# Kernel tuning notes

Hardware: AMD Instinct MI355X
Metric: run time of the kernel (lower is better)

The kernel has to match this reference:

```python
import jax, jax.numpy as jnp
import numpy as np

MARGIN = 1.0
EPS = 1e-6  # torch F.pairwise_distance default eps
B, C, D = 16384, 1000, 1024


def setup_inputs() -> dict:
    key = jax.random.key(0)
    k1, k2, k3 = jax.random.split(key, 3)
    inputs = jax.random.normal(k1, (B, D), dtype=jnp.float32)
    labels = jax.random.randint(k2, (B,), 0, C, dtype=jnp.int64)
    target = jax.random.normal(k3, (C, D), dtype=jnp.float32)
    return {"inputs": inputs, "labels": labels, "target": target}


def _pairdist(a, b):
    # torch F.pairwise_distance(p=2): ||a - b + eps||_2 along last dim
    d = a - b + EPS
    return jnp.sqrt(jnp.sum(d * d, axis=-1))


def reference(inputs, labels, target):
    # --- negative mining: full [B, C] distance matrix via GEMM identity ---
    # (eps is a uniform per-component shift; it does not change the argmin in practice,
    #  and mining indices are non-differentiable anyway)
    x2 = jnp.sum(inputs * inputs, axis=-1, keepdims=True)          # [B, 1]
    t2 = jnp.sum(target * target, axis=-1)                          # [C]
    d2 = x2 - 2.0 * (inputs @ target.T) + t2[None, :]               # [B, C]
    d2 = jnp.maximum(d2, 0.0)
    # exclude the anchor's own class (tx == anchor_label skipped in torch loop)
    own = jax.nn.one_hot(labels, C, dtype=jnp.bool_)                 # [B, C]
    d2 = jnp.where(own, jnp.inf, d2)
    neg_idx = jnp.argmin(d2, axis=-1)                                # [B]

    positive = target[labels]                                        # [B, D]
    negative = target[neg_idx]                                       # [B, D]

    d_ap = _pairdist(inputs, positive)                               # [B]
    d_an = _pairdist(inputs, negative)                               # [B]
    per_anchor = jnp.maximum(d_ap - d_an + MARGIN, 0.0)
    # every anchor forms a valid triplet (C > 1), so total/valid == mean
    return jnp.mean(per_anchor)
```

## Files before the change

kernel.cpp:

```cpp
#include <hip/hip_runtime.h>
#include <hip/hip_bf16.h>

#define NB 16384
#define NC 1000
#define NCP 1024
#define ND 1024
#define BM 128
#define BN 256
#define KSTEPS 32
#define NCB 4

typedef __attribute__((ext_vector_type(8))) short bf16x8;
typedef __attribute__((ext_vector_type(4))) float f32x4;

typedef __attribute__((address_space(1))) const void GV;
typedef __attribute__((address_space(3))) void LV;

__device__ __forceinline__ unsigned short f2bf(float f) {
  union { float f; unsigned u; } c; c.f = f;
  unsigned b = c.u;
  return (unsigned short)((b + 0x7fffu + ((b >> 16) & 1u)) >> 16);
}
__device__ __forceinline__ unsigned pk2(float lo, float hi) {
  return ((unsigned)f2bf(hi) << 16) | (unsigned)f2bf(lo);
}

__global__ __launch_bounds__(256) void prep_kernel(const float* __restrict__ Tf,
                                                   unsigned short* __restrict__ Tb,
                                                   float* __restrict__ t2) {
  const int c = blockIdx.x;
  const int tid = threadIdx.x;
  if (c >= NC) {
    ushort4 z; z.x = z.y = z.z = z.w = 0;
    ((ushort4*)(Tb + (size_t)c * ND))[tid] = z;
    if (tid == 0) t2[c] = 1e30f;
    return;
  }
  float4 v = ((const float4*)(Tf + (size_t)c * ND))[tid];
  float ss = v.x * v.x + v.y * v.y + v.z * v.z + v.w * v.w;
  ushort4 o;
  o.x = f2bf(v.x); o.y = f2bf(v.y); o.z = f2bf(v.z); o.w = f2bf(v.w);
  ((ushort4*)(Tb + (size_t)c * ND))[tid] = o;
  #pragma unroll
  for (int m = 1; m < 64; m <<= 1) ss += __shfl_xor(ss, m, 64);
  __shared__ float red[4];
  if ((tid & 63) == 0) red[tid >> 6] = ss;
  __syncthreads();
  if (tid == 0) t2[c] = red[0] + red[1] + red[2] + red[3];
}

__global__ __launch_bounds__(256) void prepx_kernel(const float* __restrict__ X,
                                                    unsigned short* __restrict__ Xb,
                                                    float* __restrict__ x2) {
  const int r = blockIdx.x;
  const int tid = threadIdx.x;
  float4 v = ((const float4*)(X + (size_t)r * ND))[tid];
  float ss = v.x * v.x + v.y * v.y + v.z * v.z + v.w * v.w;
  ushort4 o;
  o.x = f2bf(v.x); o.y = f2bf(v.y); o.z = f2bf(v.z); o.w = f2bf(v.w);
  ((ushort4*)(Xb + (size_t)r * ND))[tid] = o;
  #pragma unroll
  for (int m = 1; m < 64; m <<= 1) ss += __shfl_xor(ss, m, 64);
  __shared__ float red[4];
  if ((tid & 63) == 0) red[tid >> 6] = ss;
  __syncthreads();
  if (tid == 0) x2[r] = red[0] + red[1] + red[2] + red[3];
}

__global__ __launch_bounds__(512, 4) void mine4_kernel(
    const unsigned short* __restrict__ Xb, const int* __restrict__ labels,
    const unsigned short* __restrict__ Tb, const float* __restrict__ t2g,
    float* __restrict__ slab, float2* __restrict__ pairs) {
  __shared__ char sA[2][BM * 64];
  __shared__ char sB[2][BN * 64];
  __shared__ int sLab[BM];
  __shared__ float2 sMin[BM][4];

  const int tid = threadIdx.x;
  const int lane = tid & 63;
  const int wid = tid >> 6;
  const int l15 = lane & 15, l4 = lane >> 4;
  const int wr = wid >> 2, wc = wid & 3;

  const int bid = (int)blockIdx.x;
  const int wgid = (bid & 7) * 64 + (bid >> 3);
  const int rb = wgid >> 2, cb = wgid & 3;
  const int rowbase = rb * BM, colbase = cb * BN;

  if (tid < BM) sLab[tid] = labels[rowbase + tid];

  auto stage = [&](int buf, int ks) {
    {
      const int o = tid * 16;
      const char* src = (const char*)Xb + (size_t)(rowbase + (o >> 6)) * 2048 + ks * 64 + (o & 63);
      __builtin_amdgcn_global_load_lds((GV*)src, (LV*)(sA[buf] + o), 16, 0, 0);
    }
    #pragma unroll
    for (int i = 0; i < 2; ++i) {
      const int o = i * 8192 + tid * 16;
      const char* src = (const char*)Tb + (size_t)(colbase + (o >> 6)) * 2048 + ks * 64 + (o & 63);
      __builtin_amdgcn_global_load_lds((GV*)src, (LV*)(sB[buf] + o), 16, 0, 0);
    }
  };

  f32x4 acc[4][4] = {};
  stage(0, 0);
  int cur = 0;
  for (int ks = 0; ks < KSTEPS; ++ks) {
    __syncthreads();
    if (ks + 1 < KSTEPS) stage(cur ^ 1, ks + 1);
    const char* pa = sA[cur];
    const char* pb = sB[cur];
    bf16x8 af[4];
    #pragma unroll
    for (int m = 0; m < 4; ++m)
      af[m] = *(const bf16x8*)(pa + ((wr * 64 + m * 16 + l15) * 64 + l4 * 16));
    #pragma unroll
    for (int n = 0; n < 4; ++n) {
      bf16x8 bfr = *(const bf16x8*)(pb + ((wc * 64 + n * 16 + l15) * 64 + l4 * 16));
      #pragma unroll
      for (int m = 0; m < 4; ++m)
        acc[m][n] = __builtin_amdgcn_mfma_f32_16x16x32_bf16(af[m], bfr, acc[m][n], 0, 0, 0);
    }
    cur ^= 1;
  }

  float t2v[4];
  #pragma unroll
  for (int n = 0; n < 4; ++n) t2v[n] = t2g[colbase + wc * 64 + n * 16 + l15];

  #pragma unroll
  for (int m = 0; m < 4; ++m) {
    #pragma unroll
    for (int j = 0; j < 4; ++j) {
      const int rowl = wr * 64 + m * 16 + l4 * 4 + j;
      const int lab = sLab[rowl];
      float bv = 3.0e38f; int bi = 0x7fffffff;
      #pragma unroll
      for (int n = 0; n < 4; ++n) {
        const int col = colbase + wc * 64 + n * 16 + l15;
        const float sc = t2v[n] - 2.0f * acc[m][n][j];
        if (col == lab) slab[rowbase + rowl] = sc;
        const float sce = (col == lab) ? 3.2e38f : sc;
        if (sce < bv || (sce == bv && col < bi)) { bv = sce; bi = col; }
      }
      #pragma unroll
      for (int mk = 1; mk < 16; mk <<= 1) {
        const float ov = __shfl_xor(bv, mk, 64);
        const int   oi = __shfl_xor(bi, mk, 64);
        if (ov < bv || (ov == bv && oi < bi)) { bv = ov; bi = oi; }
      }
      if (l15 == 0) sMin[rowl][wc] = make_float2(bv, __int_as_float(bi));
    }
  }
  __syncthreads();
  if (tid < BM) {
    float2 p = sMin[tid][0];
    #pragma unroll
    for (int q = 1; q < 4; ++q) {
      float2 o = sMin[tid][q];
      if (o.x < p.x || (o.x == p.x && __float_as_int(o.y) < __float_as_int(p.y))) p = o;
    }
    pairs[(size_t)(rowbase + tid) * NCB + cb] = p;
  }
}

__global__ __launch_bounds__(512, 4) void mine2_kernel(
    const float* __restrict__ X, const int* __restrict__ labels,
    const unsigned short* __restrict__ Tb, const float* __restrict__ t2g,
    float* __restrict__ x2g, float* __restrict__ slab, float2* __restrict__ pairs) {
  __shared__ char sA[2][BM * 64];
  __shared__ char sB[2][BN * 64];
  __shared__ int sLab[BM];
  __shared__ float2 sMin[BM][4];

  const int tid = threadIdx.x;
  const int lane = tid & 63;
  const int wid = tid >> 6;
  const int l15 = lane & 15, l4 = lane >> 4;
  const int wr = wid >> 2, wc = wid & 3;
  const int rb = (int)blockIdx.x >> 2, cb = (int)blockIdx.x & 3;
  const int rowbase = rb * BM, colbase = cb * BN;

  if (tid < BM) sLab[tid] = labels[rowbase + tid];

  const int arow = tid >> 2;
  const float* aptr = X + (size_t)(rowbase + arow) * ND + ((tid & 3) << 3);
  float ss = 0.0f;

  f32x4 acc[4][4] = {};
  int cur = 0;

  auto stage = [&](int buf, int ks) {
    #pragma unroll
    for (int i = 0; i < 2; ++i) {
      const int o = i * 8192 + tid * 16;
      const char* src = (const char*)Tb + (size_t)(colbase + (o >> 6)) * 2048 + ks * 64 + (o & 63);
      __builtin_amdgcn_global_load_lds((GV*)src, (LV*)(sB[buf] + o), 16, 0, 0);
    }
    float4 v0 = *(const float4*)(aptr + ks * 32);
    float4 v1 = *(const float4*)(aptr + ks * 32 + 4);
    if (cb == 0) {
      ss += v0.x * v0.x + v0.y * v0.y + v0.z * v0.z + v0.w * v0.w
          + v1.x * v1.x + v1.y * v1.y + v1.z * v1.z + v1.w * v1.w;
    }
    uint4 w;
    w.x = pk2(v0.x, v0.y); w.y = pk2(v0.z, v0.w);
    w.z = pk2(v1.x, v1.y); w.w = pk2(v1.z, v1.w);
    *(uint4*)(sA[buf] + tid * 16) = w;
  };

  stage(0, 0);
  for (int ks = 0; ks < KSTEPS; ++ks) {
    __syncthreads();
    if (ks + 1 < KSTEPS) stage(cur ^ 1, ks + 1);
    const char* pa = sA[cur];
    const char* pb = sB[cur];
    bf16x8 af[4];
    #pragma unroll
    for (int m = 0; m < 4; ++m)
      af[m] = *(const bf16x8*)(pa + ((wr * 64 + m * 16 + l15) * 64 + l4 * 16));
    #pragma unroll
    for (int n = 0; n < 4; ++n) {
      bf16x8 bfr = *(const bf16x8*)(pb + ((wc * 64 + n * 16 + l15) * 64 + l4 * 16));
      #pragma unroll
      for (int m = 0; m < 4; ++m)
        acc[m][n] = __builtin_amdgcn_mfma_f32_16x16x32_bf16(af[m], bfr, acc[m][n], 0, 0, 0);
    }
    cur ^= 1;
  }

  if (cb == 0) {
    ss += __shfl_xor(ss, 1, 64);
    ss += __shfl_xor(ss, 2, 64);
    if ((tid & 3) == 0) x2g[rowbase + arow] = ss;
  }

  float t2v[4];
  #pragma unroll
  for (int n = 0; n < 4; ++n) t2v[n] = t2g[colbase + wc * 64 + n * 16 + l15];

  #pragma unroll
  for (int m = 0; m < 4; ++m) {
    #pragma unroll
    for (int j = 0; j < 4; ++j) {
      const int rowl = wr * 64 + m * 16 + l4 * 4 + j;
      const int lab = sLab[rowl];
      float bv = 3.0e38f; int bi = 0x7fffffff;
      #pragma unroll
      for (int n = 0; n < 4; ++n) {
        const int col = colbase + wc * 64 + n * 16 + l15;
        const float sc = t2v[n] - 2.0f * acc[m][n][j];
        if (col == lab) slab[rowbase + rowl] = sc;
        const float sce = (col == lab) ? 3.2e38f : sc;
        if (sce < bv || (sce == bv && col < bi)) { bv = sce; bi = col; }
      }
      #pragma unroll
      for (int mk = 1; mk < 16; mk <<= 1) {
        const float ov = __shfl_xor(bv, mk, 64);
        const int   oi = __shfl_xor(bi, mk, 64);
        if (ov < bv || (ov == bv && oi < bi)) { bv = ov; bi = oi; }
      }
      if (l15 == 0) sMin[rowl][wc] = make_float2(bv, __int_as_float(bi));
    }
  }
  __syncthreads();
  if (tid < BM) {
    float2 p = sMin[tid][0];
    #pragma unroll
    for (int q = 1; q < 4; ++q) {
      float2 o = sMin[tid][q];
      if (o.x < p.x || (o.x == p.x && __float_as_int(o.y) < __float_as_int(p.y))) p = o;
    }
    pairs[(size_t)(rowbase + tid) * NCB + cb] = p;
  }
}

__global__ __launch_bounds__(256) void finalize_kernel(
    const float2* __restrict__ pairs, const float* __restrict__ slab,
    const float* __restrict__ x2g, float* __restrict__ out) {
  const int r = blockIdx.x * 256 + threadIdx.x;
  float2 p = pairs[(size_t)r * NCB];
  #pragma unroll
  for (int q = 1; q < NCB; ++q) {
    float2 o = pairs[(size_t)r * NCB + q];
    if (o.x < p.x || (o.x == p.x && __float_as_int(o.y) < __float_as_int(p.y))) p = o;
  }
  const float x2v = x2g[r];
  const float dap = sqrtf(fmaxf(x2v + slab[r], 0.0f));
  const float dan = sqrtf(fmaxf(x2v + p.x, 0.0f));
  float h = fmaxf(dap - dan + 1.0f, 0.0f);
  #pragma unroll
  for (int mk = 1; mk < 64; mk <<= 1) h += __shfl_xor(h, mk, 64);
  __shared__ float red[4];
  if ((threadIdx.x & 63) == 0) red[threadIdx.x >> 6] = h;
  __syncthreads();
  if (threadIdx.x == 0)
    atomicAdd(out, (red[0] + red[1] + red[2] + red[3]) * (1.0f / (float)NB));
}

extern "C" void kernel_launch(void* const* d_in, const int* in_sizes, int n_in,
                              void* d_out, int out_size, void* d_ws, size_t ws_size,
                              hipStream_t stream) {
  const float* X = (const float*)d_in[0];
  const int* labels = (const int*)d_in[1];
  const float* Tf = (const float*)d_in[2];
  float* out = (float*)d_out;

  char* ws = (char*)d_ws;
  unsigned short* Tb = (unsigned short*)ws;
  float* t2   = (float*)(ws + 2097152);
  float* x2   = (float*)(ws + 2097152 + 4096);
  float* slab = (float*)(ws + 2097152 + 4096 + 65536);
  float2* pairs = (float2*)(ws + 2097152 + 4096 + 131072);
  unsigned short* Xb = (unsigned short*)(ws + 2756608);

  const size_t NEED = 2756608u + (size_t)NB * ND * 2u;

  hipMemsetAsync(d_out, 0, sizeof(float), stream);
  prep_kernel<<<NCP, 256, 0, stream>>>(Tf, Tb, t2);
  if (ws_size >= NEED) {
    prepx_kernel<<<NB, 256, 0, stream>>>(X, Xb, x2);
    mine4_kernel<<<(NB / BM) * NCB, 512, 0, stream>>>(Xb, labels, Tb, t2, slab, pairs);
  } else {
    mine2_kernel<<<(NB / BM) * NCB, 512, 0, stream>>>(X, labels, Tb, t2, x2, slab, pairs);
  }
  finalize_kernel<<<NB / 256, 256, 0, stream>>>(pairs, slab, x2, out);
}
```

Measured before the change: 150.2 us.

## Triple-buffer LDS staging with XOR swizzle in mining GEMM kernel

Changes the mining GEMM's LDS pipeline from double to triple buffering, prefetching two k-steps ahead, and replaces __syncthreads with an explicit vmcnt wait plus s_barrier so one stage of loads stays in flight. It also XOR-swizzles the global source columns on the direct-to-LDS loads and matches that swizzle on the fragment reads to cut LDS bank conflicts. The larger LDS footprint lowers the occupancy hint from 4 to 2 blocks, and the hand-written waitcnt counts must match the number of loads issued per stage.

```diff
diff --git a/kernel.cpp b/kernel.cpp
--- a/kernel.cpp
+++ b/kernel.cpp
@@ -67,12 +67,12 @@
   if (tid == 0) x2[r] = red[0] + red[1] + red[2] + red[3];
 }
 
-__global__ __launch_bounds__(512, 4) void mine4_kernel(
+__global__ __launch_bounds__(512, 2) void mine5_kernel(
     const unsigned short* __restrict__ Xb, const int* __restrict__ labels,
     const unsigned short* __restrict__ Tb, const float* __restrict__ t2g,
     float* __restrict__ slab, float2* __restrict__ pairs) {
-  __shared__ char sA[2][BM * 64];
-  __shared__ char sB[2][BN * 64];
+  __shared__ char sA[3][BM * 64];
+  __shared__ char sB[3][BN * 64];
   __shared__ int sLab[BM];
   __shared__ float2 sMin[BM][4];
 
@@ -89,40 +89,56 @@
 
   if (tid < BM) sLab[tid] = labels[rowbase + tid];
 
+  const int ssw = ((tid >> 3) & 3) << 4;
   auto stage = [&](int buf, int ks) {
     {
       const int o = tid * 16;
-      const char* src = (const char*)Xb + (size_t)(rowbase + (o >> 6)) * 2048 + ks * 64 + (o & 63);
+      const char* src = (const char*)Xb + (size_t)(rowbase + (o >> 6)) * 2048
+                        + ks * 64 + ((o & 63) ^ ssw);
       __builtin_amdgcn_global_load_lds((GV*)src, (LV*)(sA[buf] + o), 16, 0, 0);
     }
     #pragma unroll
     for (int i = 0; i < 2; ++i) {
       const int o = i * 8192 + tid * 16;
-      const char* src = (const char*)Tb + (size_t)(colbase + (o >> 6)) * 2048 + ks * 64 + (o & 63);
+      const char* src = (const char*)Tb + (size_t)(colbase + (o >> 6)) * 2048
+                        + ks * 64 + ((o & 63) ^ ssw);
       __builtin_amdgcn_global_load_lds((GV*)src, (LV*)(sB[buf] + o), 16, 0, 0);
     }
   };
 
+  const int rsw = ((l15 >> 1) & 3) << 4;
+  const int rdcol = (l4 * 16) ^ rsw;
+
   f32x4 acc[4][4] = {};
+
   stage(0, 0);
-  int cur = 0;
+  stage(1, 1);
+  int b_cur = 0, b_nxt = 1, b_pre = 2;
+
   for (int ks = 0; ks < KSTEPS; ++ks) {
-    __syncthreads();
-    if (ks + 1 < KSTEPS) stage(cur ^ 1, ks + 1);
-    const char* pa = sA[cur];
-    const char* pb = sB[cur];
+    __builtin_amdgcn_sched_barrier(0);
+    if (ks < KSTEPS - 1)
+      asm volatile("s_waitcnt vmcnt(3) lgkmcnt(0)\n\ts_barrier" ::: "memory");
+    else
+      asm volatile("s_waitcnt vmcnt(0) lgkmcnt(0)\n\ts_barrier" ::: "memory");
+    __builtin_amdgcn_sched_barrier(0);
+
+    if (ks + 2 < KSTEPS) stage(b_pre, ks + 2);
+
+    const char* pa = sA[b_cur];
+    const char* pb = sB[b_cur];
     bf16x8 af[4];
     #pragma unroll
     for (int m = 0; m < 4; ++m)
-      af[m] = *(const bf16x8*)(pa + ((wr * 64 + m * 16 + l15) * 64 + l4 * 16));
+      af[m] = *(const bf16x8*)(pa + ((wr * 64 + m * 16 + l15) * 64 + rdcol));
     #pragma unroll
     for (int n = 0; n < 4; ++n) {
-      bf16x8 bfr = *(const bf16x8*)(pb + ((wc * 64 + n * 16 + l15) * 64 + l4 * 16));
+      bf16x8 bfr = *(const bf16x8*)(pb + ((wc * 64 + n * 16 + l15) * 64 + rdcol));
       #pragma unroll
       for (int m = 0; m < 4; ++m)
         acc[m][n] = __builtin_amdgcn_mfma_f32_16x16x32_bf16(af[m], bfr, acc[m][n], 0, 0, 0);
     }
-    cur ^= 1;
+    const int t = b_cur; b_cur = b_nxt; b_nxt = b_pre; b_pre = t;
   }
 
   float t2v[4];
@@ -321,7 +337,7 @@
   prep_kernel<<<NCP, 256, 0, stream>>>(Tf, Tb, t2);
   if (ws_size >= NEED) {
     prepx_kernel<<<NB, 256, 0, stream>>>(X, Xb, x2);
-    mine4_kernel<<<(NB / BM) * NCB, 512, 0, stream>>>(Xb, labels, Tb, t2, slab, pairs);
+    mine5_kernel<<<(NB / BM) * NCB, 512, 0, stream>>>(Xb, labels, Tb, t2, slab, pairs);
   } else {
     mine2_kernel<<<(NB / BM) * NCB, 512, 0, stream>>>(X, labels, Tb, t2, x2, slab, pairs);
   }
```

Result: no change. 151.2 us (+0.7%).
